# Kernel tuning notes

Measured on AMD Instinct MI355X. Metric: run time of the kernel, lower is better.

Reference implementation:

```python
import jax, jax.numpy as jnp
import numpy as np
from jax import lax

# ---- module constants (mirror CorrelatedSphericalField.__init__) ----
NLAT = 361
NLON = 2 * NLAT
LMAX = NLAT            # number of degrees l
MMAX = NLAT + 1        # number of orders m = nlon//2 + 1
N_LATENT = 16
T_STEPS = 8
LENGTH_SCALE = 500_000.0
TIME_SCALE = 48.0
SIGMA = 0.3
DT = 6.0
R_EARTH = 6_371_000.0
PHI = float(np.exp(-DT / TIME_SCALE))
KT = (LENGTH_SCALE / R_EARTH) ** 2 / 2.0
FOUR_PI = float(4.0 * np.pi)


def _precompute_pct():
    """Associated Legendre tensor pct[m, l, k] for InverseRealSHT,
    equiangular grid, norm='backward' (orthonormal P / sqrt(4pi)), with
    Condon-Shortley phase -- matches torch_harmonics _precompute_legpoly(inverse=True)."""
    theta = np.linspace(0.0, np.pi, NLAT)      # equiangular incl. poles
    x = np.cos(theta)
    s = np.sin(theta)
    nmax = max(MMAX, LMAX)
    vdm = np.zeros((nmax, nmax, NLAT), dtype=np.float64)  # [m, l, lat]
    vdm[0, 0] = 1.0 / np.sqrt(4.0 * np.pi)
    for m in range(1, nmax):                    # diagonal P_m^m
        vdm[m, m] = np.sqrt((2.0 * m + 1.0) / (2.0 * m)) * s * vdm[m - 1, m - 1]
    for m in range(nmax - 1):                   # P_{m+1}^m
        vdm[m, m + 1] = np.sqrt(2.0 * m + 3.0) * x * vdm[m, m]
    for l in range(2, nmax):                    # three-term recurrence, vectorized over m
        ms = np.arange(l - 1)
        a = np.sqrt((4.0 * l * l - 1.0) / (l * l - ms * ms))[:, None]
        b = np.sqrt(((l - 1.0) ** 2 - ms * ms) / (4.0 * (l - 1.0) ** 2 - 1.0))[:, None]
        vdm[ms, l] = a * (x[None, :] * vdm[ms, l - 1] - b * vdm[ms, l - 2])
    vdm[1::2] *= -1.0                           # Condon-Shortley phase
    pct = vdm[:MMAX, :LMAX] / np.sqrt(4.0 * np.pi)  # norm='backward', inverse=True
    return jnp.asarray(pct, dtype=jnp.float32)


def _make_sigma_n():
    j = np.arange(1, NLAT, dtype=np.float64)
    denom = 2.0 * np.sum((2.0 * j + 1.0) * np.exp(-KT * j * (j + 1.0)))
    F0 = np.sqrt(SIGMA ** 2 * (1.0 - PHI ** 2) / denom)
    l = np.arange(NLAT, dtype=np.float64)
    prods = np.repeat((l * (l + 1.0))[:, None], MMAX, axis=1)   # (nlat, nlat+1)
    sn = np.tril(np.exp(-KT * prods / 2.0) * F0)                # keep m <= l
    return jnp.asarray(sn, dtype=jnp.float32)


def setup_inputs() -> dict:
    key = jax.random.key(0)
    k0, k1 = jax.random.split(key)
    sigma_n = _make_sigma_n()
    # initial stationary AR(1) coefficients: (1-phi^2)^{-1/2} * sigma_n * xi0
    xi0 = jax.random.normal(k0, (N_LATENT, LMAX, MMAX, 2), dtype=jnp.float32)
    coeff0 = (1.0 - PHI ** 2) ** (-0.5) * sigma_n[None, :, :, None] * xi0
    # pre-drawn innovations for the T AR(1) updates (real/imag stacked)
    xi = jax.random.normal(k1, (T_STEPS, N_LATENT, LMAX, MMAX, 2), dtype=jnp.float32)
    pct = _precompute_pct()
    x = jnp.zeros((T_STEPS,), dtype=jnp.int32)   # only x.shape[0] is used
    return {"x": x, "sigma_n": sigma_n, "coeff0": coeff0, "xi": xi, "pct": pct}


def reference(x, sigma_n, coeff0, xi, pct):
    T = x.shape[0]
    c0 = coeff0[..., 0] + 1j * coeff0[..., 1]    # (N, L, M) complex64
    xic = xi[..., 0] + 1j * xi[..., 1]           # (T, N, L, M) complex64

    # AR(1): emit coeff BEFORE update (matches the torch loop ordering)
    def step(c, xk):
        return PHI * c + sigma_n * xk, c

    _, coeffs = lax.scan(step, c0, xic[:T])      # (T, N, L, M)

    # inverse real SHT, batched over all T steps at once:
    # xs[..., k, m] = sum_l coeff[..., l, m] * pct[m, l, k]
    re = jnp.einsum('tnlm,mlk->tnkm', coeffs.real, pct)
    im = jnp.einsum('tnlm,mlk->tnkm', coeffs.imag, pct)
    xs = re + 1j * im                            # (T, N, nlat, mmax)
    out = jnp.fft.irfft(xs, n=NLON, axis=-1, norm='forward') * FOUR_PI
    return out.reshape(T, 1, 1, N_LATENT, NLAT, NLON)
```

## Files before the change

kernel.cpp:

```cpp
#include <hip/hip_runtime.h>
#include <math.h>

#define NLATC   361
#define NLONC   722
#define MMAXC   362
#define LMAXC   361
#define NLK     16
#define TSTEPS  8
#define LCUT    128
#define MCUT    128
#define MCK     256
#define TNK     46208
#define NPAD    768
#define KPAD    384
#define PHI_F   0.8824969025845955f
#define FOURPI  12.566370614359172f
#define ASCALE  1024.0f
#define OSCALE  0.0009765625f

typedef _Float16 half8 __attribute__((ext_vector_type(8)));
typedef _Float16 half4 __attribute__((ext_vector_type(4)));
typedef _Float16 half2v __attribute__((ext_vector_type(2)));
typedef float floatx4 __attribute__((ext_vector_type(4)));

#define GLOAD16(g, l) __builtin_amdgcn_global_load_lds( \
    (const __attribute__((address_space(1))) void*)(g), \
    (__attribute__((address_space(3))) void*)(l), 16, 0, 0)

__global__ __launch_bounds__(256) void k_prep(const float* __restrict__ sigma_n,
                                              const float* __restrict__ coeff0,
                                              const float* __restrict__ xi,
                                              const float* __restrict__ pct,
                                              _Float16* __restrict__ Bf,
                                              _Float16* __restrict__ pTf,
                                              _Float16* __restrict__ cB) {
    __shared__ __align__(16) char smem[8448];
    int bid = blockIdx.x;
    int tid = threadIdx.x;

    if (bid < 256) {
        float* xiL = (float*)smem;
        int b = bid;
        int mt = b & 3, lt = (b >> 2) & 3, n = b >> 4;
        int m0 = mt * 32, l0b = lt * 32;
        int ml = tid >> 3, lg = tid & 7;
        int m  = m0 + ml;
        int l0 = l0b + lg * 4;
        int w = tid >> 6, lane = tid & 63;
        int srow = lane >> 4, schunk = (lane & 15) * 4;
        float sg[4], cr[4], ci[4];
#pragma unroll
        for (int i = 0; i < 4; ++i)
            sg[i] = sigma_n[(size_t)(l0 + i) * MMAXC + m];
        {
            const float* src = coeff0 + ((size_t)n * LMAXC + l0b) * (MMAXC * 2) + m0 * 2;
#pragma unroll
            for (int g = 0; g < 2; ++g) {
                int row = w * 8 + g * 4;
                GLOAD16(src + (size_t)(row + srow) * (MMAXC * 2) + schunk,
                        &xiL[row * 64]);
            }
        }
        __syncthreads();
#pragma unroll
        for (int i = 0; i < 4; ++i) {
            cr[i] = xiL[(lg * 4 + i) * 64 + ml * 2];
            ci[i] = xiL[(lg * 4 + i) * 64 + ml * 2 + 1];
        }
#pragma unroll
        for (int t = 0; t < TSTEPS; ++t) {
            if (t < TSTEPS - 1) {
                __syncthreads();
                const float* src = xi
                    + (((size_t)t * NLK + n) * LMAXC + l0b) * (MMAXC * 2) + m0 * 2;
#pragma unroll
                for (int g = 0; g < 2; ++g) {
                    int row = w * 8 + g * 4;
                    GLOAD16(src + (size_t)(row + srow) * (MMAXC * 2) + schunk,
                            &xiL[row * 64]);
                }
            }
            half4 hr, hi;
#pragma unroll
            for (int i = 0; i < 4; ++i) {
                hr[i] = (_Float16)(cr[i] * ASCALE);
                hi[i] = (_Float16)(ci[i] * ASCALE);
            }
            size_t rowR = ((size_t)m * 256 +       t * 16 + n) * 128 + l0;
            size_t rowI = ((size_t)m * 256 + 128 + t * 16 + n) * 128 + l0;
            *(half4*)&cB[rowR] = hr;
            *(half4*)&cB[rowI] = hi;
            if (t < TSTEPS - 1) {
                __syncthreads();
#pragma unroll
                for (int i = 0; i < 4; ++i) {
                    float xr = xiL[(lg * 4 + i) * 64 + ml * 2];
                    float xim = xiL[(lg * 4 + i) * 64 + ml * 2 + 1];
                    cr[i] = PHI_F * cr[i] + sg[i] * xr;
                    ci[i] = PHI_F * ci[i] + sg[i] * xim;
                }
            }
        }
    } else if (bid < 1024) {
        int j = bid - 256;
        int mc = tid;
        int m = mc >> 1, c = mc & 1;
        float v = 0.0f;
        if (j < NLONC) {
            int r = (m * j) % NLONC;
            float th = (float)r * (6.283185307179586f / 722.0f);
            float s, co;
            sincosf(th, &s, &co);
            float wq = (m == 0 ? 1.0f : 2.0f) * FOURPI;
            v = c ? (-wq * s) : (wq * co);
        }
        Bf[(size_t)j * 256 + mc] = (_Float16)v;
    } else {
        _Float16 (*sm)[66] = (_Float16(*)[66])smem;
        int b = bid - 1024;
        int k0 = (b % 6) * 64;
        int l0 = ((b / 6) & 1) * 64;
        int m  = b / 12;
        int tx = tid & 63, ty = tid >> 6;
#pragma unroll
        for (int i = 0; i < 16; ++i) {
            int row = ty * 16 + i;
            int k = k0 + tx;
            sm[row][tx] = (k < NLATC)
                ? (_Float16)pct[((size_t)m * LMAXC + l0 + row) * NLATC + k] : (_Float16)0.0f;
        }
        __syncthreads();
#pragma unroll
        for (int i = 0; i < 16; ++i) {
            int kr = ty * 16 + i;
            pTf[((size_t)m * KPAD + k0 + kr) * 128 + l0 + tx] = sm[tx][kr];
        }
    }
}

__global__ __launch_bounds__(256) void k_leg(const _Float16* __restrict__ cB,
                                             const _Float16* __restrict__ pTf,
                                             _Float16* __restrict__ xsTh) {
    __shared__ _Float16 As[256][32];
    __shared__ _Float16 Bs[64][32];
    int tid = threadIdx.x;
    int lin = blockIdx.y * 6 + blockIdx.x;
    int wg  = (lin & 7) * 96 + (lin >> 3);
    int k0c = (wg % 6) * 64;
    int m   = wg / 6;
    int w = tid >> 6, lane = tid & 63, m16 = lane & 15, quad = lane >> 4;
    int rA = lane >> 2;
    int cA = (lane & 3) * 8;
    floatx4 acc[4][4];
#pragma unroll
    for (int i = 0; i < 4; ++i)
#pragma unroll
        for (int j = 0; j < 4; ++j) acc[i][j] = (floatx4)(0.0f);

    int lt0 = m & ~31;
    for (int lt = lt0; lt < 128; lt += 32) {
#pragma unroll
        for (int c = 0; c < 4; ++c) {
            int rr = w * 64 + c * 16;
            GLOAD16(&cB[((size_t)m * 256 + rr + rA) * 128 + lt + cA], &As[rr][0]);
        }
        {
            int rr = w * 16;
            GLOAD16(&pTf[((size_t)m * KPAD + k0c + rr + rA) * 128 + lt + cA], &Bs[rr][0]);
        }
        __syncthreads();
        half8 a[4], b[4];
#pragma unroll
        for (int i = 0; i < 4; ++i) a[i] = *(const half8*)&As[w * 64 + i * 16 + m16][quad * 8];
#pragma unroll
        for (int j = 0; j < 4; ++j) b[j] = *(const half8*)&Bs[j * 16 + m16][quad * 8];
#pragma unroll
        for (int i = 0; i < 4; ++i)
#pragma unroll
            for (int j = 0; j < 4; ++j)
                acc[i][j] = __builtin_amdgcn_mfma_f32_16x16x32_f16(a[i], b[j], acc[i][j], 0, 0, 0);
        __syncthreads();
    }
#pragma unroll
    for (int i = 0; i < 4; ++i)
#pragma unroll
        for (int j = 0; j < 4; ++j)
#pragma unroll
            for (int reg = 0; reg < 4; ++reg) {
                int r = w * 64 + i * 16 + quad * 4 + reg;
                int c = r >> 7, tn = r & 127;
                int k = k0c + j * 16 + m16;
                if (k < NLATC)
                    xsTh[(size_t)(2 * m + c) * TNK + tn * NLATC + k] = (_Float16)acc[i][j][reg];
            }
}

__global__ __launch_bounds__(256) void k_gemm2(const _Float16* __restrict__ xsTh,
                                               const _Float16* __restrict__ Bf,
                                               float* __restrict__ C) {
    __shared__ _Float16 As[128][32];
    __shared__ _Float16 Bs[128][32];
    int tid = threadIdx.x;
    int w = tid >> 6, lane = tid & 63, m16 = lane & 15, quad = lane >> 4;
    int lin = blockIdx.y * 6 + blockIdx.x;
    int xcd = lin & 7, idx = lin >> 3;
    int wg  = (xcd < 6) ? xcd * 271 + idx : 1626 + (xcd - 6) * 270 + idx;
    int row0 = (wg / 6) * 128;
    int j0   = (wg % 6) * 128;
    int wr = (w & 1) * 64, wc = (w >> 1) * 64;
    int rB = lane >> 2, cb4 = (lane & 3) * 8;
    int tg  = tid & 15;
    int mcp = tid >> 4;
    const _Float16* aSrc = &xsTh[(size_t)(2 * mcp) * TNK + row0 + tg * 8];
    char* asBase = (char*)&As[0][0]
                 + (size_t)(8 * tg) * 64 + ((4 * mcp) ^ ((tg & 3) << 4));
    floatx4 acc[4][4];
#pragma unroll
    for (int i = 0; i < 4; ++i)
#pragma unroll
        for (int j = 0; j < 4; ++j) acc[i][j] = (floatx4)(0.0f);

    half8 pa0 = *(const half8*)(aSrc);
    half8 pa1 = *(const half8*)(aSrc + TNK);

#pragma unroll
    for (int k0 = 0; k0 < MCK; k0 += 32) {
#pragma unroll
        for (int c = 0; c < 2; ++c) {
            int rr = w * 32 + c * 16;
            GLOAD16(&Bf[(size_t)(j0 + rr + rB) * MCK + k0 + cb4], &Bs[rr][0]);
        }
#pragma unroll
        for (int e = 0; e < 8; ++e) {
            half2v p; p[0] = pa0[e]; p[1] = pa1[e];
            *(half2v*)(asBase + e * 64) = p;
        }
        __syncthreads();
        if (k0 + 32 < MCK) {
            const _Float16* p = aSrc + (size_t)(k0 + 32) * TNK;
            pa0 = *(const half8*)(p);
            pa1 = *(const half8*)(p + TNK);
        }
        half8 a[4], b[4];
#pragma unroll
        for (int i = 0; i < 4; ++i) {
            int r = wr + i * 16 + m16;
            int g = (quad ^ ((r >> 3) & 3)) << 4;
            a[i] = *(const half8*)((const char*)&As[0][0] + (size_t)r * 64 + g);
        }
#pragma unroll
        for (int j = 0; j < 4; ++j) b[j] = *(const half8*)&Bs[wc + j * 16 + m16][quad * 8];
#pragma unroll
        for (int i = 0; i < 4; ++i)
#pragma unroll
            for (int j = 0; j < 4; ++j)
                acc[i][j] = __builtin_amdgcn_mfma_f32_16x16x32_f16(a[i], b[j], acc[i][j], 0, 0, 0);
        __syncthreads();
    }
#pragma unroll
    for (int i = 0; i < 4; ++i)
#pragma unroll
        for (int j = 0; j < 4; ++j)
#pragma unroll
            for (int reg = 0; reg < 4; ++reg) {
                int row = row0 + wr + i * 16 + quad * 4 + reg;
                int col = j0 + wc + j * 16 + m16;
                if (col < NLONC)
                    C[(size_t)row * NLONC + col] = acc[i][j][reg] * OSCALE;
            }
}

extern "C" void kernel_launch(void* const* d_in, const int* in_sizes, int n_in,
                              void* d_out, int out_size, void* d_ws, size_t ws_size,
                              hipStream_t stream) {
    (void)in_sizes; (void)n_in; (void)out_size; (void)ws_size;
    const float* sigma_n = (const float*)d_in[1];
    const float* coeff0  = (const float*)d_in[2];
    const float* xi      = (const float*)d_in[3];
    const float* pct     = (const float*)d_in[4];
    float* out = (float*)d_out;

    char* ws = (char*)d_ws;
    size_t off = 0;
    _Float16* cB   = (_Float16*)(ws + off); off += (size_t)128 * 256 * 128 * 2;
    _Float16* pTf  = (_Float16*)(ws + off); off += (size_t)128 * KPAD * 128 * 2;
    _Float16* xsTh = (_Float16*)(ws + off); off += (size_t)MCK * TNK * 2;
    _Float16* Bf   = (_Float16*)(ws + off); off += (size_t)NPAD * MCK * 2;

    k_prep<<<2560, 256, 0, stream>>>(sigma_n, coeff0, xi, pct, Bf, pTf, cB);
    k_leg<<<dim3(6, 128), 256, 0, stream>>>(cB, pTf, xsTh);
    k_gemm2<<<dim3(6, 361), 256, 0, stream>>>(xsTh, Bf, out);
}
```

Before: 369.5 us.

## Double-buffer LDS tiles in k_gemm2 with manual waitcnt and barriers

The irfft GEMM kernel now keeps two LDS buffers for the A and B tiles. The next K-slice is fetched into the alternate buffer while MFMAs consume the current one, which removes one of the two block barriers per iteration. Sched_barriers and explicit s_waitcnt vmcnt/lgkmcnt counts control when the async global_load_lds and register prefetches are awaited. This doubles LDS use to 32KB per block, and correctness depends on the hand-counted vmcnt values matching the outstanding loads.

```diff
diff --git a/kernel.cpp b/kernel.cpp
--- a/kernel.cpp
+++ b/kernel.cpp
@@ -27,6 +27,12 @@
     (const __attribute__((address_space(1))) void*)(g), \
     (__attribute__((address_space(3))) void*)(l), 16, 0, 0)
 
+#define SCHEDB()  __builtin_amdgcn_sched_barrier(0)
+#define BAR()     __builtin_amdgcn_s_barrier()
+#define WAITV2()   asm volatile("s_waitcnt vmcnt(2)" ::: "memory")
+#define WAITV2L0() asm volatile("s_waitcnt vmcnt(2) lgkmcnt(0)" ::: "memory")
+#define WAITV0L0() asm volatile("s_waitcnt vmcnt(0) lgkmcnt(0)" ::: "memory")
+
 __global__ __launch_bounds__(256) void k_prep(const float* __restrict__ sigma_n,
                                               const float* __restrict__ coeff0,
                                               const float* __restrict__ xi,
@@ -198,8 +204,8 @@
 __global__ __launch_bounds__(256) void k_gemm2(const _Float16* __restrict__ xsTh,
                                                const _Float16* __restrict__ Bf,
                                                float* __restrict__ C) {
-    __shared__ _Float16 As[128][32];
-    __shared__ _Float16 Bs[128][32];
+    __shared__ _Float16 As[2][128][32];
+    __shared__ _Float16 Bs[2][128][32];
     int tid = threadIdx.x;
     int w = tid >> 6, lane = tid & 63, m16 = lane & 15, quad = lane >> 4;
     int lin = blockIdx.y * 6 + blockIdx.x;
@@ -212,7 +218,7 @@
     int tg  = tid & 15;
     int mcp = tid >> 4;
     const _Float16* aSrc = &xsTh[(size_t)(2 * mcp) * TNK + row0 + tg * 8];
-    char* asBase = (char*)&As[0][0]
+    char* asBase = (char*)&As[0][0][0]
                  + (size_t)(8 * tg) * 64 + ((4 * mcp) ^ ((tg & 3) << 4));
     floatx4 acc[4][4];
 #pragma unroll
@@ -222,40 +228,73 @@
 
     half8 pa0 = *(const half8*)(aSrc);
     half8 pa1 = *(const half8*)(aSrc + TNK);
-
-#pragma unroll
-    for (int k0 = 0; k0 < MCK; k0 += 32) {
-#pragma unroll
-        for (int c = 0; c < 2; ++c) {
-            int rr = w * 32 + c * 16;
-            GLOAD16(&Bf[(size_t)(j0 + rr + rB) * MCK + k0 + cb4], &Bs[rr][0]);
-        }
-#pragma unroll
-        for (int e = 0; e < 8; ++e) {
-            half2v p; p[0] = pa0[e]; p[1] = pa1[e];
-            *(half2v*)(asBase + e * 64) = p;
-        }
-        __syncthreads();
-        if (k0 + 32 < MCK) {
-            const _Float16* p = aSrc + (size_t)(k0 + 32) * TNK;
-            pa0 = *(const half8*)(p);
-            pa1 = *(const half8*)(p + TNK);
+    SCHEDB();
+#pragma unroll
+    for (int c = 0; c < 2; ++c) {
+        int rr = w * 32 + c * 16;
+        GLOAD16(&Bf[(size_t)(j0 + rr + rB) * MCK + cb4], &Bs[0][rr][0]);
+    }
+    SCHEDB();
+    WAITV2();
+#pragma unroll
+    for (int e = 0; e < 8; ++e) {
+        half2v p; p[0] = pa0[e]; p[1] = pa1[e];
+        *(half2v*)(asBase + e * 64) = p;
+    }
+    SCHEDB();
+    {
+        const _Float16* p = aSrc + (size_t)32 * TNK;
+        pa0 = *(const half8*)(p);
+        pa1 = *(const half8*)(p + TNK);
+    }
+    SCHEDB();
+    WAITV2L0();
+    BAR(); SCHEDB();
+
+#pragma unroll
+    for (int t = 0; t < 8; ++t) {
+        int cur = t & 1;
+        if (t < 7) {
+#pragma unroll
+            for (int c = 0; c < 2; ++c) {
+                int rr = w * 32 + c * 16;
+                GLOAD16(&Bf[(size_t)(j0 + rr + rB) * MCK + (t + 1) * 32 + cb4],
+                        &Bs[cur ^ 1][rr][0]);
+            }
+            SCHEDB();
+            WAITV2();
+#pragma unroll
+            for (int e = 0; e < 8; ++e) {
+                half2v p; p[0] = pa0[e]; p[1] = pa1[e];
+                *(half2v*)(asBase + (cur ^ 1) * 8192 + e * 64) = p;
+            }
+            SCHEDB();
+            if (t < 6) {
+                const _Float16* p = aSrc + (size_t)(t + 2) * 32 * TNK;
+                pa0 = *(const half8*)(p);
+                pa1 = *(const half8*)(p + TNK);
+            }
+            SCHEDB();
         }
         half8 a[4], b[4];
 #pragma unroll
         for (int i = 0; i < 4; ++i) {
             int r = wr + i * 16 + m16;
             int g = (quad ^ ((r >> 3) & 3)) << 4;
-            a[i] = *(const half8*)((const char*)&As[0][0] + (size_t)r * 64 + g);
-        }
-#pragma unroll
-        for (int j = 0; j < 4; ++j) b[j] = *(const half8*)&Bs[wc + j * 16 + m16][quad * 8];
+            a[i] = *(const half8*)((const char*)&As[cur][0][0] + (size_t)r * 64 + g);
+        }
+#pragma unroll
+        for (int j = 0; j < 4; ++j) b[j] = *(const half8*)&Bs[cur][wc + j * 16 + m16][quad * 8];
 #pragma unroll
         for (int i = 0; i < 4; ++i)
 #pragma unroll
             for (int j = 0; j < 4; ++j)
                 acc[i][j] = __builtin_amdgcn_mfma_f32_16x16x32_f16(a[i], b[j], acc[i][j], 0, 0, 0);
-        __syncthreads();
+        if (t < 7) {
+            if (t < 6) { WAITV2L0(); }
+            else       { WAITV0L0(); }
+            BAR(); SCHEDB();
+        }
     }
 #pragma unroll
     for (int i = 0; i < 4; ++i)
```

Result: no change. 374.0 us (+1.2%).
